# Kernel optimization log

Measured on AMD Instinct MI355X. Metric: run time of the kernel, lower is better.

The kernel has to match this reference:

```python
import jax, jax.numpy as jnp
import numpy as np

D_MODEL = 1024
NUM_HEADS = 16
HEAD_DIM = D_MODEL // NUM_HEADS


def setup_inputs() -> dict:
    key = jax.random.key(0)
    k_x, k_wqkv, k_bqkv, k_wo, k_bo = jax.random.split(key, 5)
    bound_qkv = 1.0 / np.sqrt(D_MODEL)
    x = jax.random.normal(k_x, (2, 2048, D_MODEL), dtype=jnp.float32)
    # torch nn.Linear init: U(-1/sqrt(fan_in), 1/sqrt(fan_in))
    W_qkv = jax.random.uniform(k_wqkv, (D_MODEL, 3 * D_MODEL), jnp.float32, -bound_qkv, bound_qkv)
    b_qkv = jax.random.uniform(k_bqkv, (3 * D_MODEL,), jnp.float32, -bound_qkv, bound_qkv)
    W_out = jax.random.uniform(k_wo, (D_MODEL, D_MODEL), jnp.float32, -bound_qkv, bound_qkv)
    b_out = jax.random.uniform(k_bo, (D_MODEL,), jnp.float32, -bound_qkv, bound_qkv)
    return {"x": x, "W_qkv": W_qkv, "b_qkv": b_qkv, "W_out": W_out, "b_out": b_out}


def reference(x, W_qkv, b_qkv, W_out, b_out):
    B, T, C = x.shape
    H, Dh = NUM_HEADS, HEAD_DIM
    qkv = x @ W_qkv + b_qkv                      # [B,T,3C]
    q, k, v = jnp.split(qkv, 3, axis=-1)
    # [B,T,C] -> [B,H,T,Dh]
    def to_heads(t):
        return t.reshape(B, T, H, Dh).transpose(0, 2, 1, 3)
    q, k, v = to_heads(q), to_heads(k), to_heads(v)
    scale = 1.0 / np.sqrt(Dh).astype(np.float32)
    scores = jnp.einsum("bhqd,bhkd->bhqk", q, k) * scale   # [B,H,T,T]
    weights = jax.nn.softmax(scores, axis=-1)
    attn = jnp.einsum("bhqk,bhkd->bhqd", weights, v)        # [B,H,T,Dh]
    attn = attn.transpose(0, 2, 1, 3).reshape(B, T, C)
    return attn @ W_out + b_out
```

## Files before the change

### kernel.cpp

```cpp
#include <hip/hip_runtime.h>

typedef __bf16 bf16x8 __attribute__((ext_vector_type(8)));
typedef float f32x4 __attribute__((ext_vector_type(4)));

#define MFMA16(a, b, c) __builtin_amdgcn_mfma_f32_16x16x32_bf16(a, b, c, 0, 0, 0)
#define GLDS16(g, l)                                                              \
  __builtin_amdgcn_global_load_lds((const __attribute__((address_space(1))) void*)(g), \
                                   (__attribute__((address_space(3))) void*)(l), 16, 0, 0)

__global__ __launch_bounds__(256) void cvt_bf16_kernel(const float* __restrict__ in,
                                                       __bf16* __restrict__ out, int n4) {
  int i = blockIdx.x * 256 + threadIdx.x;
  if (i < n4) {
    float4 v = ((const float4*)in)[i];
    union { __bf16 b[4]; uint2 u; } t;
    t.b[0] = (__bf16)v.x; t.b[1] = (__bf16)v.y;
    t.b[2] = (__bf16)v.z; t.b[3] = (__bf16)v.w;
    ((uint2*)out)[i] = t.u;
  }
}

__global__ __launch_bounds__(256) void transpose_w_kernel(const float* __restrict__ Wq,
                                                          __bf16* __restrict__ WqT,
                                                          const float* __restrict__ Wo,
                                                          __bf16* __restrict__ WoT) {
  const int Kd = 1024;
  int bx = blockIdx.x;
  const float* W; __bf16* WT; int Nd, n0;
  if (bx < 96) { W = Wq; WT = WqT; Nd = 3072; n0 = bx * 32; }
  else         { W = Wo; WT = WoT; Nd = 1024; n0 = (bx - 96) * 32; }
  __shared__ float tile[32][33];
  int k0 = blockIdx.y * 32;
  int tid = threadIdx.x;
  int kk = tid >> 3, nn = (tid & 7) * 4;
  float4 v = *(const float4*)&W[(size_t)(k0 + kk) * Nd + n0 + nn];
  tile[kk][nn] = v.x; tile[kk][nn + 1] = v.y;
  tile[kk][nn + 2] = v.z; tile[kk][nn + 3] = v.w;
  __syncthreads();
  int n2 = tid >> 3, k2 = (tid & 7) * 4;
  union { __bf16 b[4]; uint2 u; } t;
  t.b[0] = (__bf16)tile[k2][n2];
  t.b[1] = (__bf16)tile[k2 + 1][n2];
  t.b[2] = (__bf16)tile[k2 + 2][n2];
  t.b[3] = (__bf16)tile[k2 + 3][n2];
  *(uint2*)&WT[(size_t)(n0 + n2) * Kd + k0 + k2] = t.u;
}

template <bool OUT_F32, int NT>
__global__ __launch_bounds__(256) void gemm_kernel(const __bf16* __restrict__ A,
                                                   const __bf16* __restrict__ BT,
                                                   const float* __restrict__ bias,
                                                   void* __restrict__ Cout, int N,
                                                   int qn, float qs) {
  const int K = 1024;
  const int NJ = NT / 32;
  __shared__ __align__(16) __bf16 As[128 * 32];
  __shared__ __align__(16) __bf16 Bs[NT * 32];
  int tid = threadIdx.x;
  int wave = tid >> 6, lane = tid & 63;
  int quad = lane >> 4, l16 = lane & 15;
  int m0 = blockIdx.x * 128, n0 = blockIdx.y * NT;
  int wm = (wave >> 1) * 64, wn = (wave & 1) * (NT / 2);

  int srow = tid >> 2, scol = (tid & 3) * 8;
  const __bf16* aptr = A + (size_t)(m0 + srow) * K + scol;
  const __bf16* bptr = BT + (size_t)(n0 + srow) * K + scol;
  __bf16* asl = &As[(size_t)wave * 512];
  __bf16* bsl = &Bs[(size_t)wave * 512];

  f32x4 acc[4][NJ] = {};
  for (int k0 = 0; k0 < K; k0 += 32) {
    GLDS16(aptr + k0, asl);
    GLDS16(aptr + (size_t)64 * K + k0, asl + 2048);
    GLDS16(bptr + k0, bsl);
    if (NT == 128) GLDS16(bptr + (size_t)64 * K + k0, bsl + 2048);
    __syncthreads();
    bf16x8 af[4], bf[NJ];
    for (int i = 0; i < 4; i++)
      af[i] = *(bf16x8*)&As[(wm + i * 16 + l16) * 32 + quad * 8];
    for (int j = 0; j < NJ; j++)
      bf[j] = *(bf16x8*)&Bs[(wn + j * 16 + l16) * 32 + quad * 8];
    for (int i = 0; i < 4; i++)
      for (int j = 0; j < NJ; j++)
        acc[i][j] = MFMA16(af[i], bf[j], acc[i][j]);
    __syncthreads();
  }
  for (int j = 0; j < NJ; j++) {
    int col = n0 + wn + j * 16 + l16;
    float bv = bias[col];
    float sc = (col < qn) ? qs : 1.0f;
    for (int i = 0; i < 4; i++) {
      int rowb = m0 + wm + i * 16 + quad * 4;
      for (int r = 0; r < 4; r++) {
        float v = (acc[i][j][r] + bv) * sc;
        if (OUT_F32)
          ((float*)Cout)[(size_t)(rowb + r) * N + col] = v;
        else
          ((__bf16*)Cout)[(size_t)(rowb + r) * N + col] = (__bf16)v;
      }
    }
  }
}

__global__ __launch_bounds__(256) void transpose_v_kernel(const __bf16* __restrict__ qkv,
                                                          __bf16* __restrict__ Vt) {
  const int T = 2048, C3 = 3072;
  __shared__ __align__(16) __bf16 tile[64][72];
  int t0 = blockIdx.x * 64;
  int h = blockIdx.y, b = blockIdx.z;
  int tid = threadIdx.x;
  int tt = tid >> 2, c = (tid & 3) * 16;
  const __bf16* src = qkv + (size_t)(b * T + t0 + tt) * C3 + 2048 + h * 64 + c;
  *(uint4*)&tile[tt][c] = *(const uint4*)src;
  *(uint4*)&tile[tt][c + 8] = *(const uint4*)(src + 8);
  __syncthreads();
  int dd = tid >> 2, t2 = (tid & 3) * 16;
  union { __bf16 b_[16]; uint4 u[2]; } o;
  for (int i = 0; i < 16; i++) o.b_[i] = tile[t2 + i][dd];
  __bf16* dst = Vt + ((size_t)(b * 16 + h) * 64 + dd) * T + t0 + t2;
  *(uint4*)dst = o.u[0];
  *(uint4*)(dst + 8) = o.u[1];
}

__global__ __launch_bounds__(256) void attn_kernel(const __bf16* __restrict__ qkv,
                                                   const __bf16* __restrict__ Vt,
                                                   __bf16* __restrict__ O) {
  const int T = 2048, C3 = 3072;
  int q0 = blockIdx.x * 64;
  int h = blockIdx.y, b = blockIdx.z;
  int tid = threadIdx.x, wave = tid >> 6, lane = tid & 63;
  int quad = lane >> 4, l16 = lane & 15;

  __shared__ __align__(16) __bf16 Ks[64 * 64];
  __shared__ __align__(16) __bf16 Vts[64 * 64];
  __shared__ __align__(16) __bf16 Ps[4][16 * 72];

  const __bf16* qp = qkv + (size_t)(b * T + q0 + wave * 16 + l16) * C3 + h * 64;
  bf16x8 aq0 = *(const bf16x8*)(qp + quad * 8);
  bf16x8 aq1 = *(const bf16x8*)(qp + 32 + quad * 8);

  const __bf16* kbase = qkv + (size_t)(b * T) * C3 + 1024 + h * 64;
  const __bf16* vbase = Vt + (size_t)(b * 16 + h) * 64 * T;

  int srow = lane >> 3;
  int scol = ((lane & 7) ^ srow) * 8;
  int r0 = wave * 16 + srow;
  __bf16* kdst0 = &Ks[(size_t)(wave * 16) * 64];
  __bf16* kdst1 = &Ks[(size_t)(wave * 16 + 8) * 64];
  __bf16* vdst0 = &Vts[(size_t)(wave * 16) * 64];
  __bf16* vdst1 = &Vts[(size_t)(wave * 16 + 8) * 64];

  int xb0 = ((quad ^ (l16 & 7)) * 8);
  int xb1 = (((4 + quad) ^ (l16 & 7)) * 8);

  f32x4 o[4] = {};
  f32x4 lacc = {};
  bf16x8 ones;
  for (int i = 0; i < 8; i++) ones[i] = (__bf16)1.0f;

  for (int t0 = 0; t0 < T; t0 += 64) {
    __syncthreads();
    GLDS16(kbase + (size_t)(t0 + r0) * C3 + scol, kdst0);
    GLDS16(kbase + (size_t)(t0 + r0 + 8) * C3 + scol, kdst1);
    GLDS16(vbase + (size_t)r0 * T + t0 + scol, vdst0);
    GLDS16(vbase + (size_t)(r0 + 8) * T + t0 + scol, vdst1);
    __syncthreads();

    f32x4 s[4] = {};
    for (int ct = 0; ct < 4; ct++) {
      int row = ct * 16 + l16;
      bf16x8 bk0 = *(bf16x8*)&Ks[row * 64 + xb0];
      bf16x8 bk1 = *(bf16x8*)&Ks[row * 64 + xb1];
      s[ct] = MFMA16(aq0, bk0, s[ct]);
      s[ct] = MFMA16(aq1, bk1, s[ct]);
    }

    for (int ct = 0; ct < 4; ct++) {
      int cp = (((ct * 2 + (l16 >> 3)) ^ quad) << 3) | (l16 & 7);
      for (int r = 0; r < 4; r++) {
        float p = __builtin_amdgcn_exp2f(s[ct][r]);
        Ps[wave][(quad * 4 + r) * 72 + cp] = (__bf16)p;
      }
    }

    for (int kc = 0; kc < 2; kc++) {
      int cpb = (((kc * 4 + quad) ^ (l16 >> 2)) << 3);
      bf16x8 ap = *(bf16x8*)&Ps[wave][l16 * 72 + cpb];
      lacc = MFMA16(ap, ones, lacc);
      int xv = kc ? xb1 : xb0;
      for (int nt = 0; nt < 4; nt++) {
        bf16x8 bv = *(bf16x8*)&Vts[(nt * 16 + l16) * 64 + xv];
        o[nt] = MFMA16(ap, bv, o[nt]);
      }
    }
  }

  f32x4 inv;
  for (int r = 0; r < 4; r++) inv[r] = 1.0f / lacc[r];
  for (int nt = 0; nt < 4; nt++)
    for (int r = 0; r < 4; r++) {
      int row = q0 + wave * 16 + quad * 4 + r;
      O[(size_t)(b * T + row) * 1024 + h * 64 + nt * 16 + l16] =
          (__bf16)(o[nt][r] * inv[r]);
    }
}

extern "C" void kernel_launch(void* const* d_in, const int* in_sizes, int n_in,
                              void* d_out, int out_size, void* d_ws, size_t ws_size,
                              hipStream_t stream) {
  const float* x = (const float*)d_in[0];
  const float* W_qkv = (const float*)d_in[1];
  const float* b_qkv = (const float*)d_in[2];
  const float* W_out = (const float*)d_in[3];
  const float* b_out = (const float*)d_in[4];
  float* out = (float*)d_out;

  char* ws = (char*)d_ws;
  __bf16* WqkvT = (__bf16*)(ws);
  __bf16* WoT = (__bf16*)(ws + 6291456);
  __bf16* xb = (__bf16*)(ws + 8388608);
  __bf16* qkvb = (__bf16*)(ws + 16777216);
  __bf16* Vt = (__bf16*)(ws + 41943040);
  __bf16* attnb = xb;

  const float cs = 0.125f * 1.44269504089f;

  cvt_bf16_kernel<<<4096, 256, 0, stream>>>(x, xb, 1048576);
  transpose_w_kernel<<<dim3(128, 32), 256, 0, stream>>>(W_qkv, WqkvT, W_out, WoT);
  gemm_kernel<false, 128><<<dim3(32, 24), 256, 0, stream>>>(xb, WqkvT, b_qkv, qkvb, 3072,
                                                            1024, cs);
  transpose_v_kernel<<<dim3(32, 16, 2), 256, 0, stream>>>(qkvb, Vt);
  attn_kernel<<<dim3(32, 16, 2), 256, 0, stream>>>(qkvb, Vt, attnb);
  gemm_kernel<true, 64><<<dim3(32, 16), 256, 0, stream>>>(attnb, WoT, b_out, out, 1024,
                                                          0, 1.0f);
}
```

Baseline: 201.8 us.

## Rewrite attention kernel with 32x32 MFMA, double-buffered K/V, and register-resident P

```diff
diff --git a/kernel.cpp b/kernel.cpp
--- a/kernel.cpp
+++ b/kernel.cpp
@@ -2,11 +2,22 @@
 
 typedef __bf16 bf16x8 __attribute__((ext_vector_type(8)));
 typedef float f32x4 __attribute__((ext_vector_type(4)));
+typedef float f32x16 __attribute__((ext_vector_type(16)));
 
 #define MFMA16(a, b, c) __builtin_amdgcn_mfma_f32_16x16x32_bf16(a, b, c, 0, 0, 0)
+#define MFMA32(a, b, c) __builtin_amdgcn_mfma_f32_32x32x16_bf16(a, b, c, 0, 0, 0)
 #define GLDS16(g, l)                                                              \
   __builtin_amdgcn_global_load_lds((const __attribute__((address_space(1))) void*)(g), \
                                    (__attribute__((address_space(3))) void*)(l), 16, 0, 0)
+
+static __device__ __forceinline__ unsigned cvt_pk_bf16(float lo, float hi) {
+  unsigned r;
+  asm("v_cvt_pk_bf16_f32 %0, %1, %2" : "=v"(r) : "v"(lo), "v"(hi));
+  return r;
+}
+static __device__ __forceinline__ void permswap(unsigned& a, unsigned& b) {
+  asm("v_permlane32_swap_b32 %0, %1" : "+v"(a), "+v"(b));
+}
 
 __global__ __launch_bounds__(256) void cvt_bf16_kernel(const float* __restrict__ in,
                                                        __bf16* __restrict__ out, int n4) {
@@ -122,86 +133,122 @@
   *(uint4*)(dst + 8) = o.u[1];
 }
 
-__global__ __launch_bounds__(256) void attn_kernel(const __bf16* __restrict__ qkv,
-                                                   const __bf16* __restrict__ Vt,
-                                                   __bf16* __restrict__ O) {
+__global__ __launch_bounds__(512, 2) void attn_kernel(const __bf16* __restrict__ qkv,
+                                                      const __bf16* __restrict__ Vt,
+                                                      __bf16* __restrict__ O) {
   const int T = 2048, C3 = 3072;
-  int q0 = blockIdx.x * 64;
-  int h = blockIdx.y, b = blockIdx.z;
+  int bh = blockIdx.x * 4 + (blockIdx.y >> 2);
+  int b = bh >> 4, h = bh & 15;
+  int q0 = (((blockIdx.y & 3) << 1) | (int)blockIdx.z) * 256;
+
   int tid = threadIdx.x, wave = tid >> 6, lane = tid & 63;
-  int quad = lane >> 4, l16 = lane & 15;
-
-  __shared__ __align__(16) __bf16 Ks[64 * 64];
-  __shared__ __align__(16) __bf16 Vts[64 * 64];
-  __shared__ __align__(16) __bf16 Ps[4][16 * 72];
-
-  const __bf16* qp = qkv + (size_t)(b * T + q0 + wave * 16 + l16) * C3 + h * 64;
-  bf16x8 aq0 = *(const bf16x8*)(qp + quad * 8);
-  bf16x8 aq1 = *(const bf16x8*)(qp + 32 + quad * 8);
+  int l32 = lane & 31, hi = lane >> 5;
+
+  __shared__ __align__(16) __bf16 Ks[2][64 * 64];
+  __shared__ __align__(16) __bf16 Vs[2][64 * 64];
+
+  const __bf16* qp = qkv + (size_t)(b * T + q0 + wave * 32 + l32) * C3 + h * 64;
+  bf16x8 qf[4];
+#pragma unroll
+  for (int ds = 0; ds < 4; ds++)
+    qf[ds] = *(const bf16x8*)(qp + ds * 16 + hi * 8);
 
   const __bf16* kbase = qkv + (size_t)(b * T) * C3 + 1024 + h * 64;
   const __bf16* vbase = Vt + (size_t)(b * 16 + h) * 64 * T;
 
-  int srow = lane >> 3;
-  int scol = ((lane & 7) ^ srow) * 8;
-  int r0 = wave * 16 + srow;
-  __bf16* kdst0 = &Ks[(size_t)(wave * 16) * 64];
-  __bf16* kdst1 = &Ks[(size_t)(wave * 16 + 8) * 64];
-  __bf16* vdst0 = &Vts[(size_t)(wave * 16) * 64];
-  __bf16* vdst1 = &Vts[(size_t)(wave * 16 + 8) * 64];
-
-  int xb0 = ((quad ^ (l16 & 7)) * 8);
-  int xb1 = (((4 + quad) ^ (l16 & 7)) * 8);
-
-  f32x4 o[4] = {};
-  f32x4 lacc = {};
-  bf16x8 ones;
-  for (int i = 0; i < 8; i++) ones[i] = (__bf16)1.0f;
-
-  for (int t0 = 0; t0 < T; t0 += 64) {
+  int srow = wave * 8 + (lane >> 3);
+  int scol = ((lane & 7) ^ (lane >> 3)) * 8;
+  const __bf16* ksrc = kbase + (size_t)srow * C3 + scol;
+  const __bf16* vsrc = vbase + (size_t)srow * T + scol;
+
+  int off[2][4];
+#pragma unroll
+  for (int rb = 0; rb < 2; rb++)
+#pragma unroll
+    for (int c4 = 0; c4 < 4; c4++)
+      off[rb][c4] = (rb * 32 + l32) * 64 + (((c4 * 2 + hi) ^ (l32 & 7)) * 8);
+
+  f32x16 o[2] = {};
+  float rs = 0.0f;
+
+  GLDS16(ksrc, &Ks[0][wave * 512]);
+  GLDS16(vsrc, &Vs[0][wave * 512]);
+
+#pragma unroll 2
+  for (int t = 0; t < 32; t++) {
+    int cur = t & 1;
     __syncthreads();
-    GLDS16(kbase + (size_t)(t0 + r0) * C3 + scol, kdst0);
-    GLDS16(kbase + (size_t)(t0 + r0 + 8) * C3 + scol, kdst1);
-    GLDS16(vbase + (size_t)r0 * T + t0 + scol, vdst0);
-    GLDS16(vbase + (size_t)(r0 + 8) * T + t0 + scol, vdst1);
-    __syncthreads();
-
-    f32x4 s[4] = {};
-    for (int ct = 0; ct < 4; ct++) {
-      int row = ct * 16 + l16;
-      bf16x8 bk0 = *(bf16x8*)&Ks[row * 64 + xb0];
-      bf16x8 bk1 = *(bf16x8*)&Ks[row * 64 + xb1];
-      s[ct] = MFMA16(aq0, bk0, s[ct]);
-      s[ct] = MFMA16(aq1, bk1, s[ct]);
-    }
-
-    for (int ct = 0; ct < 4; ct++) {
-      int cp = (((ct * 2 + (l16 >> 3)) ^ quad) << 3) | (l16 & 7);
-      for (int r = 0; r < 4; r++) {
-        float p = __builtin_amdgcn_exp2f(s[ct][r]);
-        Ps[wave][(quad * 4 + r) * 72 + cp] = (__bf16)p;
+    if (t + 1 < 32) {
+      GLDS16(ksrc + (size_t)(t + 1) * 64 * C3, &Ks[cur ^ 1][wave * 512]);
+      GLDS16(vsrc + (t + 1) * 64, &Vs[cur ^ 1][wave * 512]);
+    }
+    const __bf16* ks = &Ks[cur][0];
+    const __bf16* vs = &Vs[cur][0];
+
+    bf16x8 kf[2][4];
+#pragma unroll
+    for (int kb = 0; kb < 2; kb++)
+#pragma unroll
+      for (int ds = 0; ds < 4; ds++)
+        kf[kb][ds] = *(const bf16x8*)(ks + off[kb][ds]);
+    f32x16 sT[2] = {};
+#pragma unroll
+    for (int kb = 0; kb < 2; kb++)
+#pragma unroll
+      for (int ds = 0; ds < 4; ds++)
+        sT[kb] = MFMA32(kf[kb][ds], qf[ds], sT[kb]);
+
+    bf16x8 ap[4];
+#pragma unroll
+    for (int kb = 0; kb < 2; kb++) {
+      float p[16];
+#pragma unroll
+      for (int r = 0; r < 16; r++) {
+        p[r] = __builtin_amdgcn_exp2f(sT[kb][r]);
+        rs += p[r];
       }
-    }
-
-    for (int kc = 0; kc < 2; kc++) {
-      int cpb = (((kc * 4 + quad) ^ (l16 >> 2)) << 3);
-      bf16x8 ap = *(bf16x8*)&Ps[wave][l16 * 72 + cpb];
-      lacc = MFMA16(ap, ones, lacc);
-      int xv = kc ? xb1 : xb0;
-      for (int nt = 0; nt < 4; nt++) {
-        bf16x8 bv = *(bf16x8*)&Vts[(nt * 16 + l16) * 64 + xv];
-        o[nt] = MFMA16(ap, bv, o[nt]);
+#pragma unroll
+      for (int hf = 0; hf < 2; hf++) {
+        unsigned w0 = cvt_pk_bf16(p[hf * 8 + 0], p[hf * 8 + 1]);
+        unsigned w1 = cvt_pk_bf16(p[hf * 8 + 2], p[hf * 8 + 3]);
+        unsigned w2 = cvt_pk_bf16(p[hf * 8 + 4], p[hf * 8 + 5]);
+        unsigned w3 = cvt_pk_bf16(p[hf * 8 + 6], p[hf * 8 + 7]);
+        permswap(w0, w2);
+        permswap(w1, w3);
+        union { unsigned u[4]; bf16x8 v; } pk;
+        pk.u[0] = w0; pk.u[1] = w1; pk.u[2] = w2; pk.u[3] = w3;
+        ap[kb * 2 + hf] = pk.v;
       }
     }
-  }
-
-  f32x4 inv;
-  for (int r = 0; r < 4; r++) inv[r] = 1.0f / lacc[r];
-  for (int nt = 0; nt < 4; nt++)
-    for (int r = 0; r < 4; r++) {
-      int row = q0 + wave * 16 + quad * 4 + r;
-      O[(size_t)(b * T + row) * 1024 + h * 64 + nt * 16 + l16] =
-          (__bf16)(o[nt][r] * inv[r]);
+
+    bf16x8 vf[2][4];
+#pragma unroll
+    for (int db = 0; db < 2; db++)
+#pragma unroll
+      for (int ks2 = 0; ks2 < 4; ks2++)
+        vf[db][ks2] = *(const bf16x8*)(vs + off[db][ks2]);
+#pragma unroll
+    for (int db = 0; db < 2; db++)
+#pragma unroll
+      for (int ks2 = 0; ks2 < 4; ks2++)
+        o[db] = MFMA32(ap[ks2], vf[db][ks2], o[db]);
+  }
+
+  unsigned xu = __float_as_uint(rs), yu = __float_as_uint(rs);
+  permswap(xu, yu);
+  float inv = 1.0f / (__uint_as_float(xu) + __uint_as_float(yu));
+  float invv[16];
+#pragma unroll
+  for (int r = 0; r < 16; r++)
+    invv[r] = __shfl(inv, (r & 3) + 8 * (r >> 2) + 4 * hi);
+
+  __bf16* ob = O + (size_t)(b * T + q0 + wave * 32) * 1024 + h * 64 + l32;
+#pragma unroll
+  for (int db = 0; db < 2; db++)
+#pragma unroll
+    for (int r = 0; r < 16; r++) {
+      int row = (r & 3) + 8 * (r >> 2) + 4 * hi;
+      ob[(size_t)row * 1024 + db * 32] = (__bf16)(o[db][r] * invv[r]);
     }
 }
 
@@ -230,7 +277,7 @@
   gemm_kernel<false, 128><<<dim3(32, 24), 256, 0, stream>>>(xb, WqkvT, b_qkv, qkvb, 3072,
                                                             1024, cs);
   transpose_v_kernel<<<dim3(32, 16, 2), 256, 0, stream>>>(qkvb, Vt);
-  attn_kernel<<<dim3(32, 16, 2), 256, 0, stream>>>(qkvb, Vt, attnb);
+  attn_kernel<<<dim3(8, 16, 2), 512, 0, stream>>>(qkvb, Vt, attnb);
   gemm_kernel<true, 64><<<dim3(32, 16), 256, 0, stream>>>(attnb, WoT, b_out, out, 1024,
                                                           0, 1.0f);
 }
```

After: 183.6 us. 9.0% less time.
